# Kernel tuning notes

Measured on AMD Instinct MI355X. Metric: run time of the kernel, lower is better.

The kernel has to match this reference:

```python
import jax, jax.numpy as jnp
import numpy as np
import math

D, H, L, V, F, B, S = 1024, 16, 4, 32000, 4096, 1, 2048
HD = D // H
LN_EPS = 1e-5


def _alibi_slopes(n_heads):
    # power-of-2 case from the torch code
    start = 2.0 ** (-2.0 ** (-(math.log2(n_heads) - 3)))
    return np.array([start * (start ** i) for i in range(n_heads)], dtype=np.float32)


def setup_inputs() -> dict:
    key = jax.random.key(0)
    ks = jax.random.split(key, 10)
    sc = 0.02
    return {
        "input_ids": jax.random.randint(ks[0], (B, S), 0, V, dtype=jnp.int64 if jax.config.jax_enable_x64 else jnp.int32),
        "emb": jax.random.normal(ks[1], (V, D), jnp.float32) * sc,
        "alibi_slopes": jnp.asarray(_alibi_slopes(H)),
        "Wq": jax.random.normal(ks[2], (L, D, D), jnp.float32) * sc,
        "Wk": jax.random.normal(ks[3], (L, D, D), jnp.float32) * sc,
        "Wv": jax.random.normal(ks[4], (L, D, D), jnp.float32) * sc,
        "Wo": jax.random.normal(ks[5], (L, D, D), jnp.float32) * sc,
        "W1": jax.random.normal(ks[6], (L, F, D), jnp.float32) * sc,
        "b1": jnp.zeros((L, F), jnp.float32),
        "W2": jax.random.normal(ks[7], (L, D, F), jnp.float32) * sc,
        "b2": jnp.zeros((L, D), jnp.float32),
        "g1": jnp.ones((L, D), jnp.float32),
        "beta1": jnp.zeros((L, D), jnp.float32),
        "g2": jnp.ones((L, D), jnp.float32),
        "beta2": jnp.zeros((L, D), jnp.float32),
        "gf": jnp.ones((D,), jnp.float32),
        "bf": jnp.zeros((D,), jnp.float32),
    }


def _layernorm(x, g, b):
    m = jnp.mean(x, axis=-1, keepdims=True)
    v = jnp.var(x, axis=-1, keepdims=True)
    return (x - m) * jax.lax.rsqrt(v + LN_EPS) * g + b


def _forward(input_ids, emb, alibi_slopes, Wq, Wk, Wv, Wo, W1, b1, W2, b2,
             g1, beta1, g2, beta2, gf, bf):
    x = emb[input_ids]  # [B, S, D]
    pos = jnp.arange(S, dtype=jnp.float32)
    dist = pos[None, :] - pos[:, None]          # [S, S], entry (i, j) = j - i
    causal = dist <= 0                           # tril mask
    bias = alibi_slopes[None, :, None, None] * dist  # [1, H, S, S]
    scale = 1.0 / math.sqrt(HD)

    def layer(x, p):
        wq, wk, wv, wo, w1, bb1, w2, bb2, gg1, be1, gg2, be2 = p
        h = _layernorm(x, gg1, be1)
        q = jnp.einsum('bsd,ed->bse', h, wq).reshape(B, S, H, HD).transpose(0, 2, 1, 3)
        k = jnp.einsum('bsd,ed->bse', h, wk).reshape(B, S, H, HD).transpose(0, 2, 1, 3)
        v = jnp.einsum('bsd,ed->bse', h, wv).reshape(B, S, H, HD).transpose(0, 2, 1, 3)
        scores = jnp.einsum('bhqd,bhkd->bhqk', q, k) * scale
        scores = scores - bias
        scores = jnp.where(causal, scores, -jnp.inf)
        w = jax.nn.softmax(scores, axis=-1)
        out = jnp.einsum('bhqk,bhkd->bhqd', w, v)
        out = out.transpose(0, 2, 1, 3).reshape(B, S, D)
        out = jnp.einsum('bsd,ed->bse', out, wo)
        x = x + out
        h2 = _layernorm(x, gg2, be2)
        ff = jax.nn.gelu(jnp.einsum('bsd,fd->bsf', h2, w1) + bb1, approximate=False)
        ff = jnp.einsum('bsf,df->bsd', ff, w2) + bb2
        return x + ff, None

    params = (Wq, Wk, Wv, Wo, W1, b1, W2, b2, g1, beta1, g2, beta2)
    x, _ = jax.lax.scan(layer, x, params)
    x = _layernorm(x, gf, bf)
    logits = jnp.einsum('bsd,vd->bsv', x, emb)  # tied lm_head
    return logits


def reference(input_ids, emb, alibi_slopes, Wq, Wk, Wv, Wo, W1, b1, W2, b2,
              g1, beta1, g2, beta2, gf, bf):
    return _forward(input_ids, emb, alibi_slopes, Wq, Wk, Wv, Wo, W1, b1, W2, b2,
                    g1, beta1, g2, beta2, gf, bf)
```

## Files before the change

kernel.cpp:

```cpp
#include <hip/hip_runtime.h>
#include <hip/hip_bf16.h>

typedef unsigned int u32;
typedef unsigned short u16;
typedef __attribute__((ext_vector_type(8))) __bf16 bf16x8;
typedef __attribute__((ext_vector_type(8))) unsigned short u16x8;
typedef __attribute__((ext_vector_type(4))) float f32x4;

#define SEQ 2048

__device__ __forceinline__ float b2f(u16 u) {
  union { u32 i; float f; } x; x.i = ((u32)u) << 16; return x.f;
}
__device__ __forceinline__ u16 f2b(float f) {
  u32 u = __float_as_uint(f);
  u = (u + 0x7fffu + ((u >> 16) & 1u)) >> 16;
  return (u16)u;
}
__device__ __forceinline__ void gload_lds16(const void* g, void* l) {
  __builtin_amdgcn_global_load_lds((const __attribute__((address_space(1))) u32*)g,
                                   (__attribute__((address_space(3))) u32*)l, 16, 0, 0);
}

struct CvtArgs {
  const float* src[7];
  u16* dst[7];
  u32 beg[8];
  u32 total;
};

__global__ __launch_bounds__(256) void cvt_all(CvtArgs a)
{
  for (u32 i = blockIdx.x * 256 + threadIdx.x; i < a.total; i += gridDim.x * 256) {
    int s = 0;
#pragma unroll
    for (int k = 1; k < 7; ++k) s += (i >= a.beg[k]);
    const u32 li = i - a.beg[s];
    const float* in = a.src[s];
    const float4 f0 = ((const float4*)in)[(size_t)li * 2];
    const float4 f1 = ((const float4*)in)[(size_t)li * 2 + 1];
    union { bf16x8 b; u16x8 u; } r;
    r.b[0] = (__bf16)f0.x; r.b[1] = (__bf16)f0.y;
    r.b[2] = (__bf16)f0.z; r.b[3] = (__bf16)f0.w;
    r.b[4] = (__bf16)f1.x; r.b[5] = (__bf16)f1.y;
    r.b[6] = (__bf16)f1.z; r.b[7] = (__bf16)f1.w;
    u16* d;
    if (s < 3) {
      const u32 layer = li >> 17;
      const u32 rem = li & 131071u;
      d = a.dst[s] + ((size_t)layer * 393216u + rem) * 8;
    } else {
      d = a.dst[s] + (size_t)li * 8;
    }
    *(u16x8*)d = r.u;
  }
}

__global__ __launch_bounds__(512, 2) void gemm256(
    const u16* __restrict__ A, const u16* __restrict__ Bt,
    float* __restrict__ C, int N, int K)
{
  __shared__ u16 As[2][256 * 64];
  __shared__ u16 Bs[2][256 * 64];
  const int tid = threadIdx.x;
  const int lane = tid & 63;
  const int wid = tid >> 6;
  const int wr = wid >> 2;
  const int wc = wid & 3;

  const int T = (int)gridDim.x;
  const int bid = (int)blockIdx.x;
  const int q8 = T >> 3, r8 = T & 7;
  const int xcd = bid & 7, base = bid >> 3;
  const int swz = (xcd < r8 ? xcd * (q8 + 1) : r8 * (q8 + 1) + (xcd - r8) * q8) + base;
  const int m0 = (swz & 7) * 256;
  const int n0 = (swz >> 3) * 256;

  f32x4 acc[8][4] = {};

  const int srow = tid >> 3;
  const int sgr = (tid & 7) ^ (srow & 7);
  const u16* gA = A + (size_t)(m0 + srow) * K + sgr * 8;
  const u16* gB = Bt + (size_t)(n0 + srow) * K + sgr * 8;
  const int dwave = wid * 512;

  const int co0 = (((lane >> 4)) ^ (lane & 7)) * 8;
  const int co1 = (((lane >> 4) + 4) ^ (lane & 7)) * 8;
  const int raA = (wr * 128 + (lane & 15)) * 64;
  const int raB = (wc * 64 + (lane & 15)) * 64;

  const int nk = K >> 6;

#pragma unroll
  for (int c = 0; c < 4; ++c) {
    gload_lds16(gA + (size_t)(c * 64) * K, &As[0][c * 4096 + dwave]);
    gload_lds16(gB + (size_t)(c * 64) * K, &Bs[0][c * 4096 + dwave]);
  }
#pragma unroll
  for (int c = 0; c < 4; ++c) {
    gload_lds16(gA + (size_t)(c * 64) * K + 64, &As[1][c * 4096 + dwave]);
    gload_lds16(gB + (size_t)(c * 64) * K + 64, &Bs[1][c * 4096 + dwave]);
  }
  asm volatile("s_waitcnt vmcnt(8)" ::: "memory");
  __builtin_amdgcn_s_barrier();
  __builtin_amdgcn_sched_barrier(0);

#pragma unroll 2
  for (int t = 0; t < nk; ++t) {
    const int cb = t & 1;
    const u16* Acur = &As[cb][0];
    const u16* Bcur = &Bs[cb][0];

    bf16x8 bf[4][2];
#pragma unroll
    for (int n = 0; n < 4; ++n) {
      const int ro = raB + n * 16 * 64;
      bf[n][0] = *(const bf16x8*)&Bcur[ro + co0];
      bf[n][1] = *(const bf16x8*)&Bcur[ro + co1];
    }
#pragma unroll
    for (int p = 0; p < 4; ++p) {
      bf16x8 af[2][2];
#pragma unroll
      for (int mm = 0; mm < 2; ++mm) {
        const int ro = raA + (p * 32 + mm * 16) * 64;
        af[mm][0] = *(const bf16x8*)&Acur[ro + co0];
        af[mm][1] = *(const bf16x8*)&Acur[ro + co1];
      }
      __builtin_amdgcn_s_setprio(1);
#pragma unroll
      for (int mm = 0; mm < 2; ++mm)
#pragma unroll
        for (int n = 0; n < 4; ++n) {
          acc[p * 2 + mm][n] = __builtin_amdgcn_mfma_f32_16x16x32_bf16(af[mm][0], bf[n][0], acc[p * 2 + mm][n], 0, 0, 0);
          acc[p * 2 + mm][n] = __builtin_amdgcn_mfma_f32_16x16x32_bf16(af[mm][1], bf[n][1], acc[p * 2 + mm][n], 0, 0, 0);
        }
      __builtin_amdgcn_s_setprio(0);
    }

    __builtin_amdgcn_s_barrier();
    if (t + 2 < nk) {
      const size_t kto = (size_t)(t + 2) * 64;
      u16* Anx = &As[cb][0];
      u16* Bnx = &Bs[cb][0];
#pragma unroll
      for (int c = 0; c < 4; ++c) {
        gload_lds16(gA + (size_t)(c * 64) * K + kto, Anx + c * 4096 + dwave);
        gload_lds16(gB + (size_t)(c * 64) * K + kto, Bnx + c * 4096 + dwave);
      }
      asm volatile("s_waitcnt vmcnt(8)" ::: "memory");
    } else if (t + 1 < nk) {
      asm volatile("s_waitcnt vmcnt(0)" ::: "memory");
    }
    __builtin_amdgcn_s_barrier();
    __builtin_amdgcn_sched_barrier(0);
  }

  const int crow = m0 + wr * 128 + ((lane >> 4) << 2);
  const int ccol = n0 + wc * 64 + (lane & 15);
#pragma unroll
  for (int m = 0; m < 8; ++m)
#pragma unroll
    for (int n = 0; n < 4; ++n)
#pragma unroll
      for (int j = 0; j < 4; ++j)
        C[(size_t)(crow + m * 16 + j) * N + ccol + n * 16] = acc[m][n][j];
}

template <int EPI>
__global__ __launch_bounds__(256, 2) void gemm128p(
    const u16* __restrict__ A, const u16* __restrict__ Bt,
    void* __restrict__ C0, void* __restrict__ C1, void* __restrict__ C2,
    const float* __restrict__ bias, int N, int K)
{
  __shared__ u16 As[2][128 * 64];
  __shared__ u16 Bs[2][128 * 64];
  const int tid = threadIdx.x;
  const int lane = tid & 63;
  const int wid = tid >> 6;
  const int wr = wid >> 1;
  const int wc = wid & 1;

  const int T = (int)gridDim.x;
  const int bid = (int)blockIdx.x;
  const int q8 = T >> 3, r8 = T & 7;
  const int xcd = bid & 7, base = bid >> 3;
  const int swz = (xcd < r8 ? xcd * (q8 + 1) : r8 * (q8 + 1) + (xcd - r8) * q8) + base;
  const int m0 = (swz & 15) * 128;
  const int n0 = (swz >> 4) * 128;

  const int kchunk = K / (int)gridDim.z;
  const int kbeg = (int)blockIdx.z * kchunk;
  const int nk = kchunk >> 6;

  f32x4 acc[4][4] = {};

  const int srow = tid >> 3;
  const int sgr = (tid & 7) ^ (srow & 7);
  const u16* gA = A + (size_t)(m0 + srow) * K + kbeg + sgr * 8;
  const u16* gB = Bt + (size_t)(n0 + srow) * K + kbeg + sgr * 8;
  const int dwave = wid * 512;

  const int co0 = (((lane >> 4)) ^ (lane & 7)) * 8;
  const int co1 = (((lane >> 4) + 4) ^ (lane & 7)) * 8;
  const int raA = (wr * 64 + (lane & 15)) * 64;
  const int raB = (wc * 64 + (lane & 15)) * 64;

#pragma unroll
  for (int c = 0; c < 4; ++c) {
    gload_lds16(gA + (size_t)(c * 32) * K, &As[0][c * 2048 + dwave]);
    gload_lds16(gB + (size_t)(c * 32) * K, &Bs[0][c * 2048 + dwave]);
  }
#pragma unroll
  for (int c = 0; c < 4; ++c) {
    gload_lds16(gA + (size_t)(c * 32) * K + 64, &As[1][c * 2048 + dwave]);
    gload_lds16(gB + (size_t)(c * 32) * K + 64, &Bs[1][c * 2048 + dwave]);
  }
  asm volatile("s_waitcnt vmcnt(8)" ::: "memory");
  __builtin_amdgcn_s_barrier();
  __builtin_amdgcn_sched_barrier(0);

#pragma unroll 2
  for (int t = 0; t < nk; ++t) {
    const int cb = t & 1;
    const u16* Acur = &As[cb][0];
    const u16* Bcur = &Bs[cb][0];

    bf16x8 bf[4][2];
#pragma unroll
    for (int n = 0; n < 4; ++n) {
      const int ro = raB + n * 16 * 64;
      bf[n][0] = *(const bf16x8*)&Bcur[ro + co0];
      bf[n][1] = *(const bf16x8*)&Bcur[ro + co1];
    }
#pragma unroll
    for (int p = 0; p < 4; ++p) {
      bf16x8 af[2];
      {
        const int ro = raA + p * 16 * 64;
        af[0] = *(const bf16x8*)&Acur[ro + co0];
        af[1] = *(const bf16x8*)&Acur[ro + co1];
      }
      __builtin_amdgcn_s_setprio(1);
#pragma unroll
      for (int n = 0; n < 4; ++n) {
        acc[p][n] = __builtin_amdgcn_mfma_f32_16x16x32_bf16(af[0], bf[n][0], acc[p][n], 0, 0, 0);
        acc[p][n] = __builtin_amdgcn_mfma_f32_16x16x32_bf16(af[1], bf[n][1], acc[p][n], 0, 0, 0);
      }
      __builtin_amdgcn_s_setprio(0);
    }

    __builtin_amdgcn_s_barrier();
    if (t + 2 < nk) {
      const size_t kto = (size_t)(t + 2) * 64;
      u16* Anx = &As[cb][0];
      u16* Bnx = &Bs[cb][0];
#pragma unroll
      for (int c = 0; c < 4; ++c) {
        gload_lds16(gA + (size_t)(c * 32) * K + kto, Anx + c * 2048 + dwave);
        gload_lds16(gB + (size_t)(c * 32) * K + kto, Bnx + c * 2048 + dwave);
      }
      asm volatile("s_waitcnt vmcnt(8)" ::: "memory");
    } else if (t + 1 < nk) {
      asm volatile("s_waitcnt vmcnt(0)" ::: "memory");
    }
    __builtin_amdgcn_s_barrier();
    __builtin_amdgcn_sched_barrier(0);
  }

  const int z = (int)blockIdx.z;
#pragma unroll
  for (int m = 0; m < 4; ++m) {
    const int rowb = m0 + wr * 64 + m * 16 + ((lane >> 4) << 2);
#pragma unroll
    for (int n = 0; n < 4; ++n) {
      const int col = n0 + wc * 64 + n * 16 + (lane & 15);
#pragma unroll
      for (int j = 0; j < 4; ++j) {
        const int r = rowb + j;
        float v = acc[m][n][j];
        if (EPI == 0) {
          float* outp = (float*)(z == 0 ? C0 : C1);
          outp[(size_t)r * N + col] = v;
        } else if (EPI == 1) {
          const int which = col >> 10;
          const int ci = col & 1023;
          u16* outp = (u16*)((which == 0) ? C0 : (which == 1) ? C1 : C2);
          outp[((size_t)(ci >> 6) * SEQ + r) * 64 + (ci & 63)] = f2b(v);
        } else {
          float xx = v + bias[col];
          float ge = 0.5f * xx * (1.0f + erff(xx * 0.70710678118654752f));
          ((u16*)C0)[(size_t)r * N + col] = f2b(ge);
        }
      }
    }
  }
}

__global__ __launch_bounds__(256) void gemm_f32b(
    const u16* __restrict__ A, const float* __restrict__ Bt,
    float* __restrict__ C0, int N, int K)
{
  __shared__ u16 As[128 * 32];
  __shared__ u16 Bs[128 * 32];
  const int tid = threadIdx.x;
  const int lane = tid & 63;
  const int w = tid >> 6;
  const int wr = w >> 1;
  const int wc = w & 1;

  const int T = (int)gridDim.x;
  const int bid = (int)blockIdx.x;
  const int q8 = T >> 3, r8 = T & 7;
  const int xcd = bid & 7, base = bid >> 3;
  int swz = (xcd < r8 ? xcd * (q8 + 1) : r8 * (q8 + 1) + (xcd - r8) * q8) + base;
  const int m0 = (swz & 15) * 128;
  const int n0 = (swz >> 4) * 128;

  f32x4 acc[4][4] = {};
  const u16* ga0 = A + (size_t)(m0 + w * 32 + (lane >> 2)) * K + (lane & 3) * 8;
  u16* la = &As[(w * 32) * 32];
  const float* gb32 = Bt + (size_t)(n0 + (tid >> 1)) * K + (tid & 1) * 16;
  u16* lbw = &Bs[(tid >> 1) * 32 + (tid & 1) * 16];

  for (int kt = 0; kt < K; kt += 32) {
    __syncthreads();
    gload_lds16(ga0 + kt, la);
    gload_lds16(ga0 + kt + 16 * K, la + 16 * 32);
    {
      const float4 f0 = *(const float4*)(gb32 + kt);
      const float4 f1 = *(const float4*)(gb32 + kt + 4);
      const float4 f2 = *(const float4*)(gb32 + kt + 8);
      const float4 f3 = *(const float4*)(gb32 + kt + 12);
      union { bf16x8 b; u16x8 u; } lo, hi;
      lo.b[0] = (__bf16)f0.x; lo.b[1] = (__bf16)f0.y;
      lo.b[2] = (__bf16)f0.z; lo.b[3] = (__bf16)f0.w;
      lo.b[4] = (__bf16)f1.x; lo.b[5] = (__bf16)f1.y;
      lo.b[6] = (__bf16)f1.z; lo.b[7] = (__bf16)f1.w;
      hi.b[0] = (__bf16)f2.x; hi.b[1] = (__bf16)f2.y;
      hi.b[2] = (__bf16)f2.z; hi.b[3] = (__bf16)f2.w;
      hi.b[4] = (__bf16)f3.x; hi.b[5] = (__bf16)f3.y;
      hi.b[6] = (__bf16)f3.z; hi.b[7] = (__bf16)f3.w;
      *(u16x8*)lbw = lo.u;
      *(u16x8*)(lbw + 8) = hi.u;
    }
    asm volatile("s_waitcnt vmcnt(0)" ::: "memory");
    __syncthreads();
    bf16x8 af[4], bfr[4];
#pragma unroll
    for (int m = 0; m < 4; ++m)
      af[m] = *(const bf16x8*)&As[(wr * 64 + m * 16 + (lane & 15)) * 32 + (lane >> 4) * 8];
#pragma unroll
    for (int n = 0; n < 4; ++n)
      bfr[n] = *(const bf16x8*)&Bs[(wc * 64 + n * 16 + (lane & 15)) * 32 + (lane >> 4) * 8];
#pragma unroll
    for (int m = 0; m < 4; ++m)
#pragma unroll
      for (int n = 0; n < 4; ++n)
        acc[m][n] = __builtin_amdgcn_mfma_f32_16x16x32_bf16(af[m], bfr[n], acc[m][n], 0, 0, 0);
  }

#pragma unroll
  for (int m = 0; m < 4; ++m) {
    const int rowb = m0 + wr * 64 + m * 16 + ((lane >> 4) << 2);
#pragma unroll
    for (int n = 0; n < 4; ++n) {
      const int col = n0 + wc * 64 + n * 16 + (lane & 15);
#pragma unroll
      for (int j = 0; j < 4; ++j)
        C0[(size_t)(rowb + j) * N + col] = acc[m][n][j];
    }
  }
}

__global__ __launch_bounds__(256) void ln_kernel(const float* __restrict__ x,
    const float* __restrict__ g, const float* __restrict__ b, u16* __restrict__ out)
{
  const int row = blockIdx.x;
  const int tid = threadIdx.x;
  const float4 v = ((const float4*)(x + (size_t)row * 1024))[tid];
  float s = v.x + v.y + v.z + v.w;
  float sq = v.x * v.x + v.y * v.y + v.z * v.z + v.w * v.w;
#pragma unroll
  for (int o = 1; o < 64; o <<= 1) { s += __shfl_xor(s, o); sq += __shfl_xor(sq, o); }
  __shared__ float ss[4], ssq[4];
  if ((tid & 63) == 0) { ss[tid >> 6] = s; ssq[tid >> 6] = sq; }
  __syncthreads();
  s = ss[0] + ss[1] + ss[2] + ss[3];
  sq = ssq[0] + ssq[1] + ssq[2] + ssq[3];
  const float mean = s * (1.0f / 1024.0f);
  const float var = sq * (1.0f / 1024.0f) - mean * mean;
  const float rstd = rsqrtf(var + 1e-5f);
  const int c = tid * 4;
  u16* o4 = out + (size_t)row * 1024 + c;
  const float4 gg = ((const float4*)g)[tid];
  const float4 bb = ((const float4*)b)[tid];
  o4[0] = f2b((v.x - mean) * rstd * gg.x + bb.x);
  o4[1] = f2b((v.y - mean) * rstd * gg.y + bb.y);
  o4[2] = f2b((v.z - mean) * rstd * gg.z + bb.z);
  o4[3] = f2b((v.w - mean) * rstd * gg.w + bb.w);
}

__global__ __launch_bounds__(256) void ln_res(float* __restrict__ x,
    const float* __restrict__ p0, const float* __restrict__ p1,
    const float* __restrict__ bias,
    const float* __restrict__ g, const float* __restrict__ b,
    u16* __restrict__ out)
{
  const int row = blockIdx.x;
  const int tid = threadIdx.x;
  const size_t off = (size_t)row * 1024;
  float4 v = ((const float4*)(x + off))[tid];
  const float4 a0 = ((const float4*)(p0 + off))[tid];
  const float4 a1 = ((const float4*)(p1 + off))[tid];
  v.x += a0.x + a1.x; v.y += a0.y + a1.y;
  v.z += a0.z + a1.z; v.w += a0.w + a1.w;
  if (bias != nullptr) {
    const float4 bi = ((const float4*)bias)[tid];
    v.x += bi.x; v.y += bi.y; v.z += bi.z; v.w += bi.w;
  }
  ((float4*)(x + off))[tid] = v;
  float s = v.x + v.y + v.z + v.w;
  float sq = v.x * v.x + v.y * v.y + v.z * v.z + v.w * v.w;
#pragma unroll
  for (int o = 1; o < 64; o <<= 1) { s += __shfl_xor(s, o); sq += __shfl_xor(sq, o); }
  __shared__ float ss[4], ssq[4];
  if ((tid & 63) == 0) { ss[tid >> 6] = s; ssq[tid >> 6] = sq; }
  __syncthreads();
  s = ss[0] + ss[1] + ss[2] + ss[3];
  sq = ssq[0] + ssq[1] + ssq[2] + ssq[3];
  const float mean = s * (1.0f / 1024.0f);
  const float var = sq * (1.0f / 1024.0f) - mean * mean;
  const float rstd = rsqrtf(var + 1e-5f);
  const int c = tid * 4;
  u16* o4 = out + off + c;
  const float4 gg = ((const float4*)g)[tid];
  const float4 bb = ((const float4*)b)[tid];
  o4[0] = f2b((v.x - mean) * rstd * gg.x + bb.x);
  o4[1] = f2b((v.y - mean) * rstd * gg.y + bb.y);
  o4[2] = f2b((v.z - mean) * rstd * gg.z + bb.z);
  o4[3] = f2b((v.w - mean) * rstd * gg.w + bb.w);
}

__global__ __launch_bounds__(256) void gather_kernel(const int* __restrict__ ids,
    const float* __restrict__ emb, float* __restrict__ x)
{
  const int srow = blockIdx.x;
  const int tid = threadIdx.x;
  const int id = ids[srow];
  ((float4*)(x + (size_t)srow * 1024))[tid] =
      ((const float4*)(emb + (size_t)id * 1024))[tid];
}

__global__ __launch_bounds__(256) void attn_kernel(
    const u16* __restrict__ q, const u16* __restrict__ k, const u16* __restrict__ v,
    const float* __restrict__ slopes, u16* __restrict__ out)
{
  const int bid = (int)blockIdx.x;
  const int swz = (bid & 7) * 32 + (bid >> 3);
  const int h = swz >> 4;
  const int q0 = (swz & 15) * 128;
  const int tid = threadIdx.x;
  const int lane = tid & 63;
  const int w = tid >> 6;
  const float slope = slopes[h];

  __shared__ u16 Ks[2][64 * 32];
  __shared__ u16 Vt[64][72];
  __shared__ u16 Pl[4][32][72];

  const u16* qb = q + ((size_t)h * SEQ + q0 + w * 32) * 64;
  bf16x8 qf[2][2];
#pragma unroll
  for (int m = 0; m < 2; ++m)
#pragma unroll
    for (int kk = 0; kk < 2; ++kk)
      qf[m][kk] = *(const bf16x8*)(qb + (m * 16 + (lane & 15)) * 64 + kk * 32 + (lane >> 4) * 8);

  f32x4 o_acc[2][4] = {};
  float mrun[2][4], lrun[2][4];
#pragma unroll
  for (int m = 0; m < 2; ++m)
#pragma unroll
    for (int j = 0; j < 4; ++j) { mrun[m][j] = -1e30f; lrun[m][j] = 0.0f; }

  const int ntiles = (q0 >> 6) + 2;
  const int wmaxrow = q0 + w * 32 + 31;

  const int kkp = w >> 1, halfp = w & 1;
  const u16* gk0 = k + ((size_t)h * SEQ + halfp * 32 + (lane >> 2)) * 64 + kkp * 32 + (lane & 3) * 8;
  u16* lk = &Ks[kkp][(halfp * 32) * 32];
  const u16* gv0 = v + ((size_t)h * SEQ + lane) * 64 + w * 16;

  for (int t = 0; t < ntiles; ++t) {
    const int j0 = t << 6;
    __syncthreads();
    gload_lds16(gk0 + (size_t)j0 * 64, lk);
    gload_lds16(gk0 + (size_t)(j0 + 16) * 64, lk + 16 * 32);
    {
      const u16* gvp = gv0 + (size_t)j0 * 64;
      u16x8 v0 = *(const u16x8*)gvp;
      u16x8 v1 = *(const u16x8*)(gvp + 8);
      const int d0 = w * 16;
#pragma unroll
      for (int i = 0; i < 8; ++i) Vt[d0 + i][lane] = v0[i];
#pragma unroll
      for (int i = 0; i < 8; ++i) Vt[d0 + 8 + i][lane] = v1[i];
    }
    asm volatile("s_waitcnt vmcnt(0)" ::: "memory");
    __syncthreads();

    if (wmaxrow >= j0) {
      f32x4 s[2][4] = {};
      __builtin_amdgcn_s_setprio(1);
#pragma unroll
      for (int kk = 0; kk < 2; ++kk) {
        bf16x8 kf[4];
#pragma unroll
        for (int n = 0; n < 4; ++n)
          kf[n] = *(const bf16x8*)&Ks[kk][(n * 16 + (lane & 15)) * 32 + (lane >> 4) * 8];
#pragma unroll
        for (int m = 0; m < 2; ++m)
#pragma unroll
          for (int n = 0; n < 4; ++n)
            s[m][n] = __builtin_amdgcn_mfma_f32_16x16x32_bf16(qf[m][kk], kf[n], s[m][n], 0, 0, 0);
      }
      __builtin_amdgcn_s_setprio(0);
      const int rq = q0 + w * 32 + ((lane >> 4) << 2);
      const int ck = j0 + (lane & 15);
#pragma unroll
      for (int m = 0; m < 2; ++m) {
#pragma unroll
        for (int j = 0; j < 4; ++j) {
          const int qi = rq + m * 16 + j;
          float mx = -1e30f;
#pragma unroll
          for (int n = 0; n < 4; ++n) {
            const int kj = ck + n * 16;
            float val = s[m][n][j] * 0.125f - slope * (float)(kj - qi);
            val = (kj <= qi) ? val : -1e30f;
            s[m][n][j] = val;
            mx = fmaxf(mx, val);
          }
#pragma unroll
          for (int o = 1; o < 16; o <<= 1) mx = fmaxf(mx, __shfl_xor(mx, o));
          const float mnew = fmaxf(mrun[m][j], mx);
          const float alpha = __expf(mrun[m][j] - mnew);
          mrun[m][j] = mnew;
          float rs = 0.0f;
          const int prow = m * 16 + ((lane >> 4) << 2) + j;
#pragma unroll
          for (int n = 0; n < 4; ++n) {
            const float p = __expf(s[m][n][j] - mnew);
            rs += p;
            Pl[w][prow][n * 16 + (lane & 15)] = f2b(p);
          }
#pragma unroll
          for (int o = 1; o < 16; o <<= 1) rs += __shfl_xor(rs, o);
          lrun[m][j] = lrun[m][j] * alpha + rs;
#pragma unroll
          for (int n = 0; n < 4; ++n) o_acc[m][n][j] *= alpha;
        }
      }
      __builtin_amdgcn_s_setprio(1);
#pragma unroll
      for (int kk = 0; kk < 2; ++kk) {
        bf16x8 pf[2], vf[4];
#pragma unroll
        for (int m = 0; m < 2; ++m)
          pf[m] = *(const bf16x8*)&Pl[w][m * 16 + (lane & 15)][kk * 32 + (lane >> 4) * 8];
#pragma unroll
        for (int n = 0; n < 4; ++n)
          vf[n] = *(const bf16x8*)&Vt[n * 16 + (lane & 15)][kk * 32 + (lane >> 4) * 8];
#pragma unroll
        for (int m = 0; m < 2; ++m)
#pragma unroll
          for (int n = 0; n < 4; ++n)
            o_acc[m][n] = __builtin_amdgcn_mfma_f32_16x16x32_bf16(pf[m], vf[n], o_acc[m][n], 0, 0, 0);
      }
      __builtin_amdgcn_s_setprio(0);
    }
  }

#pragma unroll
  for (int m = 0; m < 2; ++m) {
    const int sbase = q0 + w * 32 + m * 16 + ((lane >> 4) << 2);
#pragma unroll
    for (int n = 0; n < 4; ++n) {
      const int d = h * 64 + n * 16 + (lane & 15);
#pragma unroll
      for (int j = 0; j < 4; ++j)
        out[(size_t)(sbase + j) * 1024 + d] = f2b(o_acc[m][n][j] / lrun[m][j]);
    }
  }
}

extern "C" void kernel_launch(void* const* d_in, const int* in_sizes, int n_in,
                              void* d_out, int out_size, void* d_ws, size_t ws_size,
                              hipStream_t stream)
{
  (void)in_sizes; (void)n_in; (void)out_size;
  const int* ids = (const int*)d_in[0];
  const float* emb = (const float*)d_in[1];
  const float* slopes = (const float*)d_in[2];
  const float* Wq = (const float*)d_in[3];
  const float* Wk = (const float*)d_in[4];
  const float* Wv = (const float*)d_in[5];
  const float* Wo = (const float*)d_in[6];
  const float* W1 = (const float*)d_in[7];
  const float* b1 = (const float*)d_in[8];
  const float* W2 = (const float*)d_in[9];
  const float* b2 = (const float*)d_in[10];
  const float* g1 = (const float*)d_in[11];
  const float* be1 = (const float*)d_in[12];
  const float* g2 = (const float*)d_in[13];
  const float* be2 = (const float*)d_in[14];
  const float* gf = (const float*)d_in[15];
  const float* bfin = (const float*)d_in[16];

  char* ob = (char*)d_out;
  float* x    = (float*)ob;
  u16* qb     = (u16*)(ob + (size_t)( 8u << 20));
  u16* kb     = (u16*)(ob + (size_t)(12u << 20));
  u16* vb     = (u16*)(ob + (size_t)(16u << 20));
  u16* attn   = (u16*)(ob + (size_t)(20u << 20));
  u16* ff     = (u16*)(ob + (size_t)(24u << 20));
  u16* Wqkv_b = (u16*)(ob + (size_t)( 40u << 20));
  u16* Wo_b   = (u16*)(ob + (size_t)( 64u << 20));
  u16* W1_b   = (u16*)(ob + (size_t)( 72u << 20));
  u16* W2_b   = (u16*)(ob + (size_t)(104u << 20));
  float* p0   = (float*)(ob + (size_t)(136u << 20));
  float* p1   = (float*)(ob + (size_t)(144u << 20));
  u16* h      = (u16*)d_ws;
  const size_t emb_b_need = (size_t)(4u << 20) + (size_t)32000 * 1024 * 2;
  const bool emb_fits = ws_size >= emb_b_need;
  u16* emb_b = (u16*)((char*)d_ws + (4u << 20));
  float* logits = (float*)d_out;

  {
    CvtArgs a;
    const u32 wsz = 4 * 1024 * 1024 / 8;
    const u32 fsz = 16 * 1024 * 1024 / 8;
    const u32 esz = 32000 * 1024 / 8;
    a.src[0] = Wq; a.dst[0] = Wqkv_b;
    a.src[1] = Wk; a.dst[1] = Wqkv_b + 1024 * 1024;
    a.src[2] = Wv; a.dst[2] = Wqkv_b + 2 * 1024 * 1024;
    a.src[3] = Wo; a.dst[3] = Wo_b;
    a.src[4] = W1; a.dst[4] = W1_b;
    a.src[5] = W2; a.dst[5] = W2_b;
    a.src[6] = emb; a.dst[6] = emb_b;
    a.beg[0] = 0;
    a.beg[1] = wsz;      a.beg[2] = 2 * wsz;  a.beg[3] = 3 * wsz;
    a.beg[4] = 4 * wsz;  a.beg[5] = 4 * wsz + fsz;  a.beg[6] = 4 * wsz + 2 * fsz;
    a.beg[7] = a.beg[6] + esz;
    a.total = emb_fits ? a.beg[7] : a.beg[6];
    cvt_all<<<2048, 256, 0, stream>>>(a);
  }

  gather_kernel<<<2048, 256, 0, stream>>>(ids, emb, x);
  ln_kernel<<<2048, 256, 0, stream>>>(x, g1, be1, h);

  for (int l = 0; l < 4; ++l) {
    const size_t wqkv = (size_t)l * 3072 * 1024;
    const size_t wo = (size_t)l * 1024 * 1024;
    const size_t wf = (size_t)l * 4096 * 1024;
    gemm128p<1><<<dim3(384, 1, 1), 256, 0, stream>>>(h, Wqkv_b + wqkv,
        qb, kb, vb, nullptr, 3072, 1024);
    attn_kernel<<<dim3(256, 1, 1), 256, 0, stream>>>(qb, kb, vb, slopes, attn);
    gemm128p<0><<<dim3(128, 1, 2), 256, 0, stream>>>(attn, Wo_b + wo,
        p0, p1, nullptr, nullptr, 1024, 1024);
    ln_res<<<2048, 256, 0, stream>>>(x, p0, p1, nullptr,
        g2 + l * 1024, be2 + l * 1024, h);
    gemm128p<2><<<dim3(512, 1, 1), 256, 0, stream>>>(h, W1_b + wf,
        ff, nullptr, nullptr, b1 + l * 4096, 4096, 1024);
    gemm128p<0><<<dim3(128, 1, 2), 256, 0, stream>>>(ff, W2_b + wf,
        p0, p1, nullptr, nullptr, 1024, 4096);
    if (l < 3) {
      ln_res<<<2048, 256, 0, stream>>>(x, p0, p1, b2 + l * 1024,
          g1 + (l + 1) * 1024, be1 + (l + 1) * 1024, h);
    } else {
      ln_res<<<2048, 256, 0, stream>>>(x, p0, p1, b2 + l * 1024, gf, bfin, h);
    }
  }

  if (emb_fits) {
    gemm256<<<dim3(1000, 1, 1), 512, 0, stream>>>(h, emb_b, logits, 32000, 1024);
  } else {
    gemm_f32b<<<dim3(4000, 1, 1), 256, 0, stream>>>(h, emb, logits, 32000, 1024);
  }
}
```

Measured before the change: 1.287 ms.

## Split Wo/W2 GEMMs four ways along K and swizzle attention K tile in LDS

The Wo and FFN-down GEMMs now launch with four K-split slices instead of two. The partials are written into one contiguous buffer indexed by blockIdx.z, and a new ln_res4 sums all four partials before the residual add and layernorm. This doubles the block count on these narrow GEMMs to fill more CUs, at the cost of extra partial-sum memory traffic. Separately, the attention kernel applies an XOR swizzle to the K tile's LDS write and read offsets to reduce LDS bank conflicts.

```diff
diff --git a/kernel.cpp b/kernel.cpp
--- a/kernel.cpp
+++ b/kernel.cpp
@@ -280,7 +280,7 @@
         const int r = rowb + j;
         float v = acc[m][n][j];
         if (EPI == 0) {
-          float* outp = (float*)(z == 0 ? C0 : C1);
+          float* outp = (float*)C0 + (size_t)z * (2048u * 1024u);
           outp[(size_t)r * N + col] = v;
         } else if (EPI == 1) {
           const int which = col >> 10;
@@ -401,9 +401,8 @@
   o4[3] = f2b((v.w - mean) * rstd * gg.w + bb.w);
 }
 
-__global__ __launch_bounds__(256) void ln_res(float* __restrict__ x,
-    const float* __restrict__ p0, const float* __restrict__ p1,
-    const float* __restrict__ bias,
+__global__ __launch_bounds__(256) void ln_res4(float* __restrict__ x,
+    const float* __restrict__ P, const float* __restrict__ bias,
     const float* __restrict__ g, const float* __restrict__ b,
     u16* __restrict__ out)
 {
@@ -411,10 +410,11 @@
   const int tid = threadIdx.x;
   const size_t off = (size_t)row * 1024;
   float4 v = ((const float4*)(x + off))[tid];
-  const float4 a0 = ((const float4*)(p0 + off))[tid];
-  const float4 a1 = ((const float4*)(p1 + off))[tid];
-  v.x += a0.x + a1.x; v.y += a0.y + a1.y;
-  v.z += a0.z + a1.z; v.w += a0.w + a1.w;
+#pragma unroll
+  for (int j = 0; j < 4; ++j) {
+    const float4 a = ((const float4*)(P + (size_t)j * 2048 * 1024 + off))[tid];
+    v.x += a.x; v.y += a.y; v.z += a.z; v.w += a.w;
+  }
   if (bias != nullptr) {
     const float4 bi = ((const float4*)bias)[tid];
     v.x += bi.x; v.y += bi.y; v.z += bi.z; v.w += bi.w;
@@ -488,9 +488,11 @@
   const int wmaxrow = q0 + w * 32 + 31;
 
   const int kkp = w >> 1, halfp = w & 1;
-  const u16* gk0 = k + ((size_t)h * SEQ + halfp * 32 + (lane >> 2)) * 64 + kkp * 32 + (lane & 3) * 8;
+  const int ksl = (lane & 3) ^ ((lane >> 2) & 3);
+  const u16* gk0 = k + ((size_t)h * SEQ + halfp * 32 + (lane >> 2)) * 64 + kkp * 32 + ksl * 8;
   u16* lk = &Ks[kkp][(halfp * 32) * 32];
   const u16* gv0 = v + ((size_t)h * SEQ + lane) * 64 + w * 16;
+  const int krd = ((lane >> 4) ^ (lane & 3)) * 8;
 
   for (int t = 0; t < ntiles; ++t) {
     const int j0 = t << 6;
@@ -518,7 +520,7 @@
         bf16x8 kf[4];
 #pragma unroll
         for (int n = 0; n < 4; ++n)
-          kf[n] = *(const bf16x8*)&Ks[kk][(n * 16 + (lane & 15)) * 32 + (lane >> 4) * 8];
+          kf[n] = *(const bf16x8*)&Ks[kk][(n * 16 + (lane & 15)) * 32 + krd];
 #pragma unroll
         for (int m = 0; m < 2; ++m)
 #pragma unroll
@@ -629,8 +631,7 @@
   u16* Wo_b   = (u16*)(ob + (size_t)( 64u << 20));
   u16* W1_b   = (u16*)(ob + (size_t)( 72u << 20));
   u16* W2_b   = (u16*)(ob + (size_t)(104u << 20));
-  float* p0   = (float*)(ob + (size_t)(136u << 20));
-  float* p1   = (float*)(ob + (size_t)(144u << 20));
+  float* P    = (float*)(ob + (size_t)(136u << 20));
   u16* h      = (u16*)d_ws;
   const size_t emb_b_need = (size_t)(4u << 20) + (size_t)32000 * 1024 * 2;
   const bool emb_fits = ws_size >= emb_b_need;
@@ -667,19 +668,19 @@
     gemm128p<1><<<dim3(384, 1, 1), 256, 0, stream>>>(h, Wqkv_b + wqkv,
         qb, kb, vb, nullptr, 3072, 1024);
     attn_kernel<<<dim3(256, 1, 1), 256, 0, stream>>>(qb, kb, vb, slopes, attn);
-    gemm128p<0><<<dim3(128, 1, 2), 256, 0, stream>>>(attn, Wo_b + wo,
-        p0, p1, nullptr, nullptr, 1024, 1024);
-    ln_res<<<2048, 256, 0, stream>>>(x, p0, p1, nullptr,
+    gemm128p<0><<<dim3(128, 1, 4), 256, 0, stream>>>(attn, Wo_b + wo,
+        P, nullptr, nullptr, nullptr, 1024, 1024);
+    ln_res4<<<2048, 256, 0, stream>>>(x, P, nullptr,
         g2 + l * 1024, be2 + l * 1024, h);
     gemm128p<2><<<dim3(512, 1, 1), 256, 0, stream>>>(h, W1_b + wf,
         ff, nullptr, nullptr, b1 + l * 4096, 4096, 1024);
-    gemm128p<0><<<dim3(128, 1, 2), 256, 0, stream>>>(ff, W2_b + wf,
-        p0, p1, nullptr, nullptr, 1024, 4096);
+    gemm128p<0><<<dim3(128, 1, 4), 256, 0, stream>>>(ff, W2_b + wf,
+        P, nullptr, nullptr, nullptr, 1024, 4096);
     if (l < 3) {
-      ln_res<<<2048, 256, 0, stream>>>(x, p0, p1, b2 + l * 1024,
+      ln_res4<<<2048, 256, 0, stream>>>(x, P, b2 + l * 1024,
           g1 + (l + 1) * 1024, be1 + (l + 1) * 1024, h);
     } else {
-      ln_res<<<2048, 256, 0, stream>>>(x, p0, p1, b2 + l * 1024, gf, bfin, h);
+      ln_res4<<<2048, 256, 0, stream>>>(x, P, b2 + l * 1024, gf, bfin, h);
     }
   }
 
```

Measured after the change: 1.235 ms. 1.04x faster.
